# Kernel tuning notes

Measured on AMD Instinct MI355X. Metric: run time of the kernel, lower is better.

## Reference

```python
import jax, jax.numpy as jnp
import numpy as np


def setup_inputs() -> dict:
    key = jax.random.key(0)
    ks = jax.random.split(key, 12)
    B, N, Din, D, K = 2, 1024, 64, 64, 24
    s = lambda fan_in: 1.0 / np.sqrt(fan_in)
    return {
        "feature": jax.random.normal(ks[0], (B, N, Din), jnp.float32),
        "xyz": jax.random.normal(ks[1], (B, N, 3), jnp.float32),
        "pw1": jax.random.uniform(ks[2], (Din, D), jnp.float32, -s(Din), s(Din)),
        "pb1": jax.random.uniform(ks[3], (D,), jnp.float32, -s(Din), s(Din)),
        "pw2": jax.random.uniform(ks[4], (D, D), jnp.float32, -s(D), s(D)),
        "pb2": jax.random.uniform(ks[5], (D,), jnp.float32, -s(D), s(D)),
        "rw": jax.random.uniform(ks[6], (3, D * D), jnp.float32, -s(3), s(3)),
        "rb": jax.random.uniform(ks[7], (D * D,), jnp.float32, -s(3), s(3)),
        "sw": jax.random.uniform(ks[8], (D, D), jnp.float32, -s(D), s(D)),
        "sb": jax.random.uniform(ks[9], (D,), jnp.float32, -s(D), s(D)),
        "knn_num": 24,
    }


def reference(feature, xyz, pw1, pb1, pw2, pb2, rw, rb, sw, sb, knn_num):
    B, N, _ = feature.shape
    D = pw2.shape[1]
    K = knn_num
    # KNN over xyz (squared euclidean distances, smallest K)
    sq = jnp.sum(xyz * xyz, axis=-1)  # [B,N]
    d2 = sq[:, :, None] + sq[:, None, :] - 2.0 * jnp.einsum('bnc,bmc->bnm', xyz, xyz)
    _, idx = jax.lax.top_k(-d2, K)  # [B,N,K]
    bidx = jnp.arange(B)[:, None, None]
    rel = xyz[bidx, idx] - xyz[:, :, None, :]  # [B,N,K,3]
    # prefix MLP: relu(Linear -> ReLU -> Linear)
    feat = jax.nn.relu(jax.nn.relu(feature @ pw1 + pb1) @ pw2 + pb2)  # [B,N,D]
    # per-edge weight generation + softmax over (K*D)
    w = (rel @ rw + rb).reshape(B, N, K * D, D)
    w = jax.nn.softmax(w, axis=-2)
    # gather neighbor features and aggregate
    gv = feat[bidx, idx].reshape(B, N, K * D)  # [B,N,K*D]
    out = jnp.einsum('bnm,bnmd->bnd', gv, w)  # [B,N,D]
    out = out @ sw + sb
    return (out, N)
```

## Files before the change

### kernel.cpp

```cpp
#include <hip/hip_runtime.h>
#include <math.h>

#define BB 2
#define NN 1024
#define DD 64
#define KK 24
#define NPTS (BB * NN)

#if __has_builtin(__builtin_amdgcn_exp2f)
#define EXP2(x) __builtin_amdgcn_exp2f(x)
#else
#define EXP2(x) exp2f(x)
#endif

typedef short short8 __attribute__((ext_vector_type(8)));
typedef float floatx16 __attribute__((ext_vector_type(16)));
typedef float floatx4 __attribute__((ext_vector_type(4)));

static __device__ __forceinline__ unsigned short bf_rne(float x) {
    unsigned u = __float_as_uint(x);
    u += 0x7FFFu + ((u >> 16) & 1u);
    return (unsigned short)(u >> 16);
}
static __device__ __forceinline__ unsigned bfpack(float hi, float lo) {
    return __builtin_amdgcn_perm(__float_as_uint(hi), __float_as_uint(lo), 0x07060302u);
}

union U8 { unsigned u[4]; short8 s8; };


__global__ __launch_bounds__(256) void prep_mlp_knn_kernel(
    const float* __restrict__ feature, const float* __restrict__ xyz,
    const float* __restrict__ pw1, const float* __restrict__ pb1,
    const float* __restrict__ pw2, const float* __restrict__ pb2,
    const float* __restrict__ rw, const float* __restrict__ rb,
    float* __restrict__ feat, int* __restrict__ idx_out,
    unsigned short* __restrict__ rwB) {
    int bid = blockIdx.x;
    int tid = threadIdx.x;

    if (bid < 512) {
        int r = tid >> 6;
        int d = tid & 63;
        int row = bid * 4 + r;
        __shared__ float s_in[4][64];
        __shared__ float s_h[4][64];
        s_in[r][d] = feature[row * 64 + d];
        __syncthreads();
        float h = pb1[d];
#pragma unroll
        for (int i = 0; i < 64; i++) h = __builtin_fmaf(s_in[r][i], pw1[i * 64 + d], h);
        h = fmaxf(h, 0.f);
        s_h[r][d] = h;
        __syncthreads();
        float f = pb2[d];
#pragma unroll
        for (int i = 0; i < 64; i++) f = __builtin_fmaf(s_h[r][i], pw2[i * 64 + d], f);
        f = fmaxf(f, 0.f);
        feat[row * 64 + d] = f;
    } else if (bid < 528) {
        const float LOG2E = 1.4426950408889634f;
        int t = (bid - 512) * 256 + tid;
        unsigned b0 = bf_rne(rw[t] * LOG2E);
        unsigned b1 = bf_rne(rw[4096 + t] * LOG2E);
        unsigned b2 = bf_rne(rw[8192 + t] * LOG2E);
        unsigned b3 = bf_rne(rb[t] * LOG2E);
        uint2 v;
        v.x = b0 | (b1 << 16);
        v.y = b2 | (b3 << 16);
        *(uint2*)(rwB + 4 * t) = v;
    } else {
        int w = tid >> 6;
        int lane = tid & 63;
        int pt = (bid - 528) * 4 + w;
        int b = pt >> 10;
        int n = pt & 1023;
        const float* xb = xyz + (size_t)b * NN * 3;
        float xn = xb[n * 3 + 0], yn = xb[n * 3 + 1], zn = xb[n * 3 + 2];
        float sqn = xn * xn + yn * yn + zn * zn;
        float dist[16];
#pragma unroll
        for (int c = 0; c < 16; c++) {
            int m = c * 64 + lane;
            float xm = xb[m * 3 + 0], ym = xb[m * 3 + 1], zm = xb[m * 3 + 2];
            float sqm = xm * xm + ym * ym + zm * zm;
            float dot = xn * xm + yn * ym + zn * zm;
            dist[c] = sqn + sqm - 2.0f * dot;
        }
        for (int r = 0; r < KK; r++) {
            float best = 3.4e38f;
            int bi = 1 << 30;
#pragma unroll
            for (int c = 0; c < 16; c++) {
                if (dist[c] < best) {
                    best = dist[c];
                    bi = c * 64 + lane;
                }
            }
#pragma unroll
            for (int off = 32; off >= 1; off >>= 1) {
                float ob = __shfl_down(best, off);
                int oi = __shfl_down(bi, off);
                if (ob < best || (ob == best && oi < bi)) {
                    best = ob;
                    bi = oi;
                }
            }
            bi = __shfl(bi, 0);
            if ((bi & 63) == lane) dist[bi >> 6] = 3.4e38f;
            if (lane == 0) idx_out[pt * KK + r] = bi;
        }
    }
}

__global__ __launch_bounds__(256, 4) void agg_kernel(const float* __restrict__ xyz,
                                                     const float* __restrict__ feat,
                                                     const int* __restrict__ idx,
                                                     const unsigned short* __restrict__ rwB,
                                                     const float* __restrict__ sw,
                                                     const float* __restrict__ sb,
                                                     float* __restrict__ out) {
    int pt = blockIdx.x;
    int b = pt >> 10;
    int n = pt & 1023;
    int tid = threadIdx.x;
    int w = tid >> 6;
    int lane = tid & 63;
    int n16 = lane & 15, q4 = lane >> 4;
    int n32 = lane & 31, h = lane >> 5;

    __shared__ unsigned short s_et[64][196];
    __shared__ unsigned short s_gv[KK * 64];
    __shared__ unsigned short s_rel4[32][4];
    __shared__ float s_pre[64];
    __shared__ float s_red[4][64];

    const float* xb = xyz + (size_t)b * NN * 3;

    if (tid < 32) {
        if (tid < KK) {
            int nb = idx[pt * KK + tid];
            s_rel4[tid][0] = bf_rne(xb[nb * 3 + 0] - xb[n * 3 + 0]);
            s_rel4[tid][1] = bf_rne(xb[nb * 3 + 1] - xb[n * 3 + 1]);
            s_rel4[tid][2] = bf_rne(xb[nb * 3 + 2] - xb[n * 3 + 2]);
            s_rel4[tid][3] = 0x3F80;
        } else {
            s_rel4[tid][0] = 0; s_rel4[tid][1] = 0; s_rel4[tid][2] = 0; s_rel4[tid][3] = 0;
        }
    }
#pragma unroll
    for (int i = 0; i < 6; i++) {
        int flat = tid + 256 * i;
        int j = flat / 24;
        int k = flat - 24 * j;
        int nb = idx[pt * KK + k];
        s_gv[flat] = bf_rne(feat[((size_t)b * NN + nb) * 64 + j]);
    }
    __syncthreads();

    short8 afrag;
    {
        unsigned a01 = 0, a23 = 0;
        if (h == 0) {
            const unsigned* p = (const unsigned*)&s_rel4[n32][0];
            a01 = p[0];
            a23 = p[1];
        }
        U8 u; u.u[0] = a01; u.u[1] = a23; u.u[2] = 0; u.u[3] = 0;
        afrag = u.s8;
    }

    floatx4 c2 = (floatx4)(0.0f);
    const floatx16 z16 = (floatx16)(0.0f);
    const unsigned ONES = 0x3F803F80u;

    for (int c = 0; c < 8; c++) {
        int nt0 = 16 * c + 4 * w;
        uint2 gb = *(const uint2*)(rwB + 4 * ((nt0 << 5) + n32));
#pragma unroll 1
        for (int t = 0; t < 4; t++) {
            int nt = nt0 + t;
            uint2 gbn = gb;
            if (t < 3) gbn = *(const uint2*)(rwB + 4 * (((nt + 1) << 5) + n32));
            short8 bfrag;
            {
                unsigned b01 = (h == 0) ? gb.x : 0u;
                unsigned b23 = (h == 0) ? gb.y : 0u;
                U8 u; u.u[0] = b01; u.u[1] = b23; u.u[2] = 0; u.u[3] = 0;
                bfrag = u.s8;
            }
            floatx16 acc = __builtin_amdgcn_mfma_f32_32x32x16_bf16(afrag, bfrag, z16, 0, 0, 0);
            int jl = (nt >> 1) - 8 * c;
            int d = ((nt & 1) << 5) + n32;
#pragma unroll
            for (int g = 0; g < 3; g++) {
                float e0 = EXP2(acc[4 * g + 0]);
                float e1 = EXP2(acc[4 * g + 1]);
                float e2 = EXP2(acc[4 * g + 2]);
                float e3 = EXP2(acc[4 * g + 3]);
                uint2 pv;
                pv.x = bfpack(e1, e0);
                pv.y = bfpack(e3, e2);
                int mm = jl * 24 + 8 * g + 4 * h;
                *(uint2*)&s_et[d][mm] = pv;
            }
            gb = gbn;
        }
        __syncthreads();
#pragma unroll
        for (int ks = 0; ks < 6; ks++) {
            int mmb = 32 * ks + 8 * q4;
            uint4 gvv = *(const uint4*)&s_gv[192 * c + mmb];
            short8 ag;
            {
                U8 u;
                u.u[0] = (n16 == 0) ? gvv.x : ((n16 == 1) ? ONES : 0u);
                u.u[1] = (n16 == 0) ? gvv.y : ((n16 == 1) ? ONES : 0u);
                u.u[2] = (n16 == 0) ? gvv.z : ((n16 == 1) ? ONES : 0u);
                u.u[3] = (n16 == 0) ? gvv.w : ((n16 == 1) ? ONES : 0u);
                ag = u.s8;
            }
            const unsigned short* ep = &s_et[16 * w + n16][mmb];
            uint2 e01 = *(const uint2*)(ep);
            uint2 e23 = *(const uint2*)(ep + 4);
            short8 bg;
            {
                U8 u; u.u[0] = e01.x; u.u[1] = e01.y; u.u[2] = e23.x; u.u[3] = e23.y;
                bg = u.s8;
            }
            c2 = __builtin_amdgcn_mfma_f32_16x16x32_bf16(ag, bg, c2, 0, 0, 0);
        }
        __syncthreads();
    }

    if (q4 == 0) s_pre[16 * w + n16] = c2[0] / c2[1];
    __syncthreads();
    float part = 0.f;
#pragma unroll
    for (int i = 0; i < 16; i++) {
        int r = 16 * w + i;
        part = __builtin_fmaf(s_pre[r], sw[r * 64 + lane], part);
    }
    s_red[w][lane] = part;
    __syncthreads();
    if (tid < 64) {
        float o = s_red[0][tid] + s_red[1][tid] + s_red[2][tid] + s_red[3][tid] + sb[tid];
        out[(size_t)pt * 64 + tid] = o;
    }
    if (pt == 0 && tid == 0) out[(size_t)NPTS * 64] = 1024.0f;
}

extern "C" void kernel_launch(void* const* d_in, const int* in_sizes, int n_in,
                              void* d_out, int out_size, void* d_ws, size_t ws_size,
                              hipStream_t stream) {
    const float* feature = (const float*)d_in[0];
    const float* xyz = (const float*)d_in[1];
    const float* pw1 = (const float*)d_in[2];
    const float* pb1 = (const float*)d_in[3];
    const float* pw2 = (const float*)d_in[4];
    const float* pb2 = (const float*)d_in[5];
    const float* rw = (const float*)d_in[6];
    const float* rb = (const float*)d_in[7];
    const float* sw = (const float*)d_in[8];
    const float* sb = (const float*)d_in[9];
    float* out = (float*)d_out;

    char* ws = (char*)d_ws;
    float* feat = (float*)(ws);
    int* idx = (int*)(ws + 524288);
    unsigned short* rwB = (unsigned short*)(ws + 720896);

    prep_mlp_knn_kernel<<<1040, 256, 0, stream>>>(feature, xyz, pw1, pb1, pw2, pb2,
                                                  rw, rb, feat, idx, rwB);
    agg_kernel<<<NPTS, 256, 0, stream>>>(xyz, feat, idx, rwB, sw, sb, out);
}
```

Measured before the change: 138.5 us.

## Double-buffer exp tile in agg kernel and store MLP features as bf16

The aggregation loop is now software-pipelined over 16 half-size chunks with a double-buffered shared exp tile. Exp generation for chunk i overlaps the second MFMA reduction of chunk i-1, with one barrier per iteration instead of two. The prefix MLP now writes its features directly as bf16, which halves the gather traffic and removes per-element rounding in the agg kernel. The shared tile shrinks per buffer, but the chunks are smaller and more of them are issued.

```diff
diff --git a/kernel.cpp b/kernel.cpp
--- a/kernel.cpp
+++ b/kernel.cpp
@@ -34,7 +34,7 @@
     const float* __restrict__ pw1, const float* __restrict__ pb1,
     const float* __restrict__ pw2, const float* __restrict__ pb2,
     const float* __restrict__ rw, const float* __restrict__ rb,
-    float* __restrict__ feat, int* __restrict__ idx_out,
+    unsigned short* __restrict__ feat_bf, int* __restrict__ idx_out,
     unsigned short* __restrict__ rwB) {
     int bid = blockIdx.x;
     int tid = threadIdx.x;
@@ -57,7 +57,7 @@
 #pragma unroll
         for (int i = 0; i < 64; i++) f = __builtin_fmaf(s_h[r][i], pw2[i * 64 + d], f);
         f = fmaxf(f, 0.f);
-        feat[row * 64 + d] = f;
+        feat_bf[row * 64 + d] = bf_rne(f);
     } else if (bid < 528) {
         const float LOG2E = 1.4426950408889634f;
         int t = (bid - 512) * 256 + tid;
@@ -113,8 +113,9 @@
     }
 }
 
+#define ETS 102
 __global__ __launch_bounds__(256, 4) void agg_kernel(const float* __restrict__ xyz,
-                                                     const float* __restrict__ feat,
+                                                     const unsigned short* __restrict__ feat_bf,
                                                      const int* __restrict__ idx,
                                                      const unsigned short* __restrict__ rwB,
                                                      const float* __restrict__ sw,
@@ -129,7 +130,7 @@
     int n16 = lane & 15, q4 = lane >> 4;
     int n32 = lane & 31, h = lane >> 5;
 
-    __shared__ unsigned short s_et[64][196];
+    __shared__ unsigned short s_et[2][64][ETS];
     __shared__ unsigned short s_gv[KK * 64];
     __shared__ unsigned short s_rel4[32][4];
     __shared__ float s_pre[64];
@@ -154,7 +155,7 @@
         int j = flat / 24;
         int k = flat - 24 * j;
         int nb = idx[pt * KK + k];
-        s_gv[flat] = bf_rne(feat[((size_t)b * NN + nb) * 64 + j]);
+        s_gv[flat] = feat_bf[((size_t)b * NN + nb) * 64 + j];
     }
     __syncthreads();
 
@@ -174,61 +175,64 @@
     const floatx16 z16 = (floatx16)(0.0f);
     const unsigned ONES = 0x3F803F80u;
 
-    for (int c = 0; c < 8; c++) {
-        int nt0 = 16 * c + 4 * w;
-        uint2 gb = *(const uint2*)(rwB + 4 * ((nt0 << 5) + n32));
-#pragma unroll 1
-        for (int t = 0; t < 4; t++) {
-            int nt = nt0 + t;
-            uint2 gbn = gb;
-            if (t < 3) gbn = *(const uint2*)(rwB + 4 * (((nt + 1) << 5) + n32));
-            short8 bfrag;
-            {
-                unsigned b01 = (h == 0) ? gb.x : 0u;
-                unsigned b23 = (h == 0) ? gb.y : 0u;
-                U8 u; u.u[0] = b01; u.u[1] = b23; u.u[2] = 0; u.u[3] = 0;
-                bfrag = u.s8;
-            }
-            floatx16 acc = __builtin_amdgcn_mfma_f32_32x32x16_bf16(afrag, bfrag, z16, 0, 0, 0);
-            int jl = (nt >> 1) - 8 * c;
-            int d = ((nt & 1) << 5) + n32;
-#pragma unroll
-            for (int g = 0; g < 3; g++) {
-                float e0 = EXP2(acc[4 * g + 0]);
-                float e1 = EXP2(acc[4 * g + 1]);
-                float e2 = EXP2(acc[4 * g + 2]);
-                float e3 = EXP2(acc[4 * g + 3]);
-                uint2 pv;
-                pv.x = bfpack(e1, e0);
-                pv.y = bfpack(e3, e2);
-                int mm = jl * 24 + 8 * g + 4 * h;
-                *(uint2*)&s_et[d][mm] = pv;
-            }
-            gb = gbn;
-        }
-        __syncthreads();
-#pragma unroll
-        for (int ks = 0; ks < 6; ks++) {
-            int mmb = 32 * ks + 8 * q4;
-            uint4 gvv = *(const uint4*)&s_gv[192 * c + mmb];
-            short8 ag;
-            {
-                U8 u;
-                u.u[0] = (n16 == 0) ? gvv.x : ((n16 == 1) ? ONES : 0u);
-                u.u[1] = (n16 == 0) ? gvv.y : ((n16 == 1) ? ONES : 0u);
-                u.u[2] = (n16 == 0) ? gvv.z : ((n16 == 1) ? ONES : 0u);
-                u.u[3] = (n16 == 0) ? gvv.w : ((n16 == 1) ? ONES : 0u);
-                ag = u.s8;
-            }
-            const unsigned short* ep = &s_et[16 * w + n16][mmb];
-            uint2 e01 = *(const uint2*)(ep);
-            uint2 e23 = *(const uint2*)(ep + 4);
-            short8 bg;
-            {
-                U8 u; u.u[0] = e01.x; u.u[1] = e01.y; u.u[2] = e23.x; u.u[3] = e23.y;
-                bg = u.s8;
-            }
-            c2 = __builtin_amdgcn_mfma_f32_16x16x32_bf16(ag, bg, c2, 0, 0, 0);
+    for (int it = 0; it <= 16; it++) {
+        if (it < 16) {
+            int buf = it & 1;
+#pragma unroll
+            for (int t = 0; t < 2; t++) {
+                int tt = 2 * w + t;
+                int Jcol = it * 256 + tt * 32 + n32;
+                uint2 gb = *(const uint2*)(rwB + 4 * Jcol);
+                short8 bfrag;
+                {
+                    unsigned b01 = (h == 0) ? gb.x : 0u;
+                    unsigned b23 = (h == 0) ? gb.y : 0u;
+                    U8 u; u.u[0] = b01; u.u[1] = b23; u.u[2] = 0; u.u[3] = 0;
+                    bfrag = u.s8;
+                }
+                floatx16 acc = __builtin_amdgcn_mfma_f32_32x32x16_bf16(afrag, bfrag, z16, 0, 0, 0);
+                int jl = tt >> 1;
+                int d = ((tt & 1) << 5) + n32;
+#pragma unroll
+                for (int g = 0; g < 3; g++) {
+                    float e0 = EXP2(acc[4 * g + 0]);
+                    float e1 = EXP2(acc[4 * g + 1]);
+                    float e2 = EXP2(acc[4 * g + 2]);
+                    float e3 = EXP2(acc[4 * g + 3]);
+                    uint2 pv;
+                    pv.x = bfpack(e1, e0);
+                    pv.y = bfpack(e3, e2);
+                    int mm = jl * 24 + 8 * g + 4 * h;
+                    *(uint2*)&s_et[buf][d][mm] = pv;
+                }
+            }
+        }
+        if (it > 0) {
+            int c = it - 1;
+            int buf = c & 1;
+#pragma unroll
+            for (int ks = 0; ks < 3; ks++) {
+                int mmb = 32 * ks + 8 * q4;
+                uint4 gvv = *(const uint4*)&s_gv[96 * c + mmb];
+                short8 ag;
+                {
+                    U8 u;
+                    u.u[0] = (n16 == 0) ? gvv.x : ((n16 == 1) ? ONES : 0u);
+                    u.u[1] = (n16 == 0) ? gvv.y : ((n16 == 1) ? ONES : 0u);
+                    u.u[2] = (n16 == 0) ? gvv.z : ((n16 == 1) ? ONES : 0u);
+                    u.u[3] = (n16 == 0) ? gvv.w : ((n16 == 1) ? ONES : 0u);
+                    ag = u.s8;
+                }
+                const unsigned short* ep = &s_et[buf][16 * w + n16][mmb];
+                uint2 e01 = *(const uint2*)(ep);
+                uint2 e23 = *(const uint2*)(ep + 4);
+                short8 bg;
+                {
+                    U8 u; u.u[0] = e01.x; u.u[1] = e01.y; u.u[2] = e23.x; u.u[3] = e23.y;
+                    bg = u.s8;
+                }
+                c2 = __builtin_amdgcn_mfma_f32_16x16x32_bf16(ag, bg, c2, 0, 0, 0);
+            }
         }
         __syncthreads();
     }
@@ -266,11 +270,11 @@
     float* out = (float*)d_out;
 
     char* ws = (char*)d_ws;
-    float* feat = (float*)(ws);
-    int* idx = (int*)(ws + 524288);
-    unsigned short* rwB = (unsigned short*)(ws + 720896);
+    unsigned short* feat_bf = (unsigned short*)(ws);
+    int* idx = (int*)(ws + 262144);
+    unsigned short* rwB = (unsigned short*)(ws + 458752);
 
     prep_mlp_knn_kernel<<<1040, 256, 0, stream>>>(feature, xyz, pw1, pb1, pw2, pb2,
-                                                  rw, rb, feat, idx, rwB);
-    agg_kernel<<<NPTS, 256, 0, stream>>>(xyz, feat, idx, rwB, sw, sb, out);
-}
+                                                  rw, rb, feat_bf, idx, rwB);
+    agg_kernel<<<NPTS, 256, 0, stream>>>(xyz, feat_bf, idx, rwB, sw, sb, out);
+}
```

Measured after the change: 202.8 us. +46.4%, slower.
